# Performance work log

Measured on AMD Instinct MI355X. Metric: run time of the kernel, lower is better.

The kernel has to match this reference:

```python
import jax, jax.numpy as jnp
import numpy as np

NUM_USERS = 100000
NUM_ITEMS = 200000
N = NUM_USERS + NUM_ITEMS
D = 64
NNZ = 5_000_000
B = 16384
N_LAYERS = 3


def setup_inputs() -> dict:
    key = jax.random.key(0)
    ks = jax.random.split(key, 7)
    users = jax.random.randint(ks[0], (B,), 0, NUM_USERS, dtype=jnp.int32)
    items = jax.random.randint(ks[1], (B,), 0, NUM_ITEMS, dtype=jnp.int32)
    edge_row = jax.random.randint(ks[2], (NNZ,), 0, N, dtype=jnp.int32)
    edge_col = jax.random.randint(ks[3], (NNZ,), 0, N, dtype=jnp.int32)
    # mimic D^-1/2 A D^-1/2 normalization scale (~1/avg_degree)
    edge_vals = jax.random.uniform(ks[4], (NNZ,), dtype=jnp.float32) * 0.06
    user_emb = jax.random.normal(ks[5], (NUM_USERS, D), dtype=jnp.float32) * 0.1
    item_emb = jax.random.normal(ks[6], (NUM_ITEMS, D), dtype=jnp.float32) * 0.1
    return {
        "users": users, "items": items,
        "edge_row": edge_row, "edge_col": edge_col, "edge_vals": edge_vals,
        "user_emb": user_emb, "item_emb": item_emb,
        "n_layers": N_LAYERS,
    }


def _spmm(edge_row, edge_col, edge_vals, x):
    # sparse [N,N] @ dense [N,D] via gather + segment_sum
    msg = x[edge_col] * edge_vals[:, None]  # [nnz, D]
    return jax.ops.segment_sum(msg, edge_row, num_segments=N)


def reference(users, items, edge_row, edge_col, edge_vals, user_emb, item_emb, n_layers):
    # LightGCN.computer(): propagate + mean over layers (running-sum form)
    all_emb = jnp.concatenate([user_emb, item_emb], axis=0)  # [N, D]
    acc = all_emb
    for _ in range(n_layers):
        all_emb = _spmm(edge_row, edge_col, edge_vals, all_emb)
        acc = acc + all_emb
    light_out = acc / (n_layers + 1)
    all_users = light_out[:NUM_USERS]
    all_items = light_out[NUM_USERS:]
    # forward(users, items): elementwise dot product
    users_emb = all_users[users]
    items_emb = all_items[items]
    gamma = jnp.sum(users_emb * items_emb, axis=1)  # [B]
    return gamma
```

## Files before the change

kernel.cpp:

```cpp
#include <hip/hip_runtime.h>
#include <hip/hip_fp16.h>
#include <hip/hip_fp8.h>

namespace {

constexpr int kUsers = 100000;
constexpr int kItems = 200000;
constexpr int kN     = kUsers + kItems;
constexpr int kD     = 64;
constexpr int kNNZ   = 5000000;
constexpr int kB     = 16384;
constexpr int kRowsPerBkt = 2048;
constexpr int kNBKT  = (kN + kRowsPerBkt - 1) / kRowsPerBkt;
constexpr int kSEPB  = 4096;
constexpr int kCap   = 40960;
constexpr int kMaxSub = 2 * kB;

typedef int   v2i __attribute__((ext_vector_type(2)));
typedef float v4f __attribute__((ext_vector_type(4)));

#if defined(__has_builtin)
#if __has_builtin(__builtin_amdgcn_cvt_pk_f32_fp8) && __has_builtin(__builtin_amdgcn_cvt_f32_fp8)
#define NATIVE_FP8 1
#endif
#endif
#ifndef NATIVE_FP8
#define NATIVE_FP8 0
#endif

constexpr float kValScale = NATIVE_FP8 ? 1.0f : 256.0f;

__device__ inline void dec8(v2i h, float* f) {
#if NATIVE_FP8
  auto a0 = __builtin_amdgcn_cvt_pk_f32_fp8(h.x, false);
  auto a1 = __builtin_amdgcn_cvt_pk_f32_fp8(h.x, true);
  auto a2 = __builtin_amdgcn_cvt_pk_f32_fp8(h.y, false);
  auto a3 = __builtin_amdgcn_cvt_pk_f32_fp8(h.y, true);
  f[0] = a0[0]; f[1] = a0[1]; f[2] = a1[0]; f[3] = a1[1];
  f[4] = a2[0]; f[5] = a2[1]; f[6] = a3[0]; f[7] = a3[1];
#else
  unsigned int ws[2] = {(unsigned int)h.x, (unsigned int)h.y};
#pragma unroll
  for (int q = 0; q < 2; ++q) {
    unsigned int w = ws[q];
    unsigned int a = ((w & 0x007f007fu) << 7) | ((w & 0x00800080u) << 8);
    unsigned int b = (((w >> 8) & 0x007f007fu) << 7) | (((w >> 8) & 0x00800080u) << 8);
    float2 e = __half22float2(*reinterpret_cast<const __half2*>(&a));
    float2 o = __half22float2(*reinterpret_cast<const __half2*>(&b));
    f[4 * q + 0] = e.x; f[4 * q + 1] = o.x; f[4 * q + 2] = e.y; f[4 * q + 3] = o.y;
  }
#endif
}

__device__ inline float dec1(unsigned char b) {
#if NATIVE_FP8
  return __builtin_amdgcn_cvt_f32_fp8((int)b, 0) * 0.015625f;
#else
  unsigned int hb = ((b & 0x7fu) << 7) | ((b & 0x80u) << 8);
  return __half2float(__ushort_as_half((unsigned short)hb)) * 4.0f;
#endif
}

__device__ inline unsigned char enc(float f) { __hip_fp8_e4m3 q(f); return q.__x; }

__device__ inline float vdec(int w) {
  return __half2float(__ushort_as_half((unsigned short)((w >> 17) & 0x7FFC))) * kValScale;
}

__global__ void zero3(int* __restrict__ gpos, int* __restrict__ mark,
                      int* __restrict__ scnt) {
  int i = blockIdx.x * blockDim.x + threadIdx.x;
  if (i < kN) mark[i] = 0;
  if (i < kNBKT + 1) gpos[i] = 0;
  if (i == 0) scnt[0] = 0;
}

__global__ void bucket_scatter(const int* __restrict__ row, const int* __restrict__ col,
                               const float* __restrict__ val, int* __restrict__ gpos,
                               int* __restrict__ tmp4, unsigned short* __restrict__ tmpr) {
  __shared__ int hcnt[4][kNBKT];
  __shared__ int lofs[kNBKT];
  __shared__ int hbase[kNBKT];
  __shared__ int lds[256];
  __shared__ int sp[kSEPB];
  __shared__ unsigned short sr[kSEPB];
  __shared__ unsigned short sb[kSEPB];
  int t = threadIdx.x;
  int wv = t >> 6;
  long base = (long)blockIdx.x * kSEPB;
  int valid = (int)min((long)kSEPB, (long)kNNZ - base);
  for (int i = t; i < kNBKT; i += 256) {
    hcnt[0][i] = 0; hcnt[1][i] = 0; hcnt[2][i] = 0; hcnt[3][i] = 0;
  }
  __syncthreads();
  int py[16], bk[16], rl[16], rk[16];
  bool ok[16];
#pragma unroll
  for (int j = 0; j < 16; ++j) {
    long i = base + j * 256 + t;
    ok[j] = (i < kNNZ);
    if (ok[j]) {
      int r = __builtin_nontemporal_load(row + i);
      int c = __builtin_nontemporal_load(col + i);
      float v = __builtin_nontemporal_load(val + i);
      bk[j] = r >> 11;
      rl[j] = r & 2047;
      unsigned short hb = __half_as_ushort(__float2half_rn(v));
      int v13 = ((int)hb + 2) >> 2;
      py[j] = c | (v13 << 19);
      rk[j] = atomicAdd(&hcnt[wv][bk[j]], 1);
    }
  }
  __syncthreads();
  int own = 0;
  if (t < kNBKT) {
    int c0 = hcnt[0][t], c1 = hcnt[1][t], c2 = hcnt[2][t], c3 = hcnt[3][t];
    hcnt[0][t] = 0; hcnt[1][t] = c0; hcnt[2][t] = c0 + c1; hcnt[3][t] = c0 + c1 + c2;
    own = c0 + c1 + c2 + c3;
  }
  lds[t] = own;
  __syncthreads();
  for (int o = 1; o < 256; o <<= 1) {
    int x = (t >= o) ? lds[t - o] : 0;
    __syncthreads();
    if (t >= o) lds[t] += x;
    __syncthreads();
  }
  if (t < kNBKT) {
    lofs[t] = lds[t] - own;
    hbase[t] = t * kCap + atomicAdd(&gpos[t], own);
  }
  __syncthreads();
#pragma unroll
  for (int j = 0; j < 16; ++j) {
    if (ok[j]) {
      int pos = lofs[bk[j]] + hcnt[wv][bk[j]] + rk[j];
      sp[pos] = py[j];
      sr[pos] = (unsigned short)rl[j];
      sb[pos] = (unsigned short)bk[j];
    }
  }
  __syncthreads();
#pragma unroll
  for (int j = 0; j < 16; ++j) {
    int pos = t + j * 256;
    if (pos < valid) {
      int b = sb[pos];
      int w = hbase[b] + (pos - lofs[b]);
      tmp4[w] = sp[pos];
      tmpr[w] = sr[pos];
    }
  }
}

__global__ __launch_bounds__(1024) void build_csr(
    const int* __restrict__ gpos, const int* __restrict__ tmp4,
    const unsigned short* __restrict__ tmpr, int* __restrict__ rowptr,
    int* __restrict__ edges) {
  __shared__ int h[kRowsPerBkt];
  __shared__ int lsum[256];
  __shared__ int gscan[256];
  int b = blockIdx.x >> 1;
  int half = blockIdx.x & 1;
  int t = threadIdx.x;
  if (t < 256) gscan[t] = (t < kNBKT) ? gpos[t] : 0;
  for (int i = t; i < kRowsPerBkt; i += 1024) h[i] = 0;
  __syncthreads();
  for (int o = 1; o < 256; o <<= 1) {
    int v = 0;
    if (t < 256 && t >= o) v = gscan[t - o];
    __syncthreads();
    if (t < 256 && t >= o) gscan[t] += v;
    __syncthreads();
  }
  int bucket_base = (b == 0) ? 0 : gscan[b - 1];
  int s = b * kCap;
  int e = s + gpos[b];
  for (int j = s + t; j < e; j += 1024) atomicAdd(&h[tmpr[j]], 1);
  __syncthreads();
  int cnt[8], pref[8];
  if (t < 256) {
    int acc = 0;
#pragma unroll
    for (int k = 0; k < 8; ++k) {
      cnt[k] = h[t * 8 + k];
      pref[k] = acc;
      acc += cnt[k];
    }
    lsum[t] = acc;
  }
  __syncthreads();
  for (int o = 1; o < 256; o <<= 1) {
    int v = 0;
    if (t < 256 && t >= o) v = lsum[t - o];
    __syncthreads();
    if (t < 256 && t >= o) lsum[t] += v;
    __syncthreads();
  }
  if (t < 256) {
    int ex = (t == 0) ? 0 : lsum[t - 1];
#pragma unroll
    for (int k = 0; k < 8; ++k) {
      int g = bucket_base + ex + pref[k];
      int r = b * kRowsPerBkt + t * 8 + k;
      if (half == 0 && r < kN) rowptr[r] = g;
      h[t * 8 + k] = g;
    }
  }
  if (blockIdx.x == 0 && t == 0) rowptr[kN] = kNNZ;
  __syncthreads();
  int lo = half << 10, hi = lo + 1024;
  for (int j = s + t; j < e; j += 1024) {
    int rl = tmpr[j];
    if (rl >= lo && rl < hi) {
      int dst = atomicAdd(&h[rl], 1);
      edges[dst] = tmp4[j];
    }
  }
}

__global__ void mark_rows(const int* __restrict__ users, const int* __restrict__ items,
                          int* __restrict__ mark) {
  int i = blockIdx.x * blockDim.x + threadIdx.x;
  if (i >= kB) return;
  mark[users[i]] = 1;
  mark[kUsers + items[i]] = 1;
}

__global__ void compact_rows(const int* __restrict__ mark, int* __restrict__ list,
                             int* __restrict__ cnt) {
  __shared__ int wbase[4];
  int t = threadIdx.x;
  int i = blockIdx.x * 256 + t;
  bool m = (i < kN) && mark[i];
  unsigned long long bal = __ballot(m);
  int wv = t >> 6, ln = t & 63;
  if (ln == 0) wbase[wv] = __popcll(bal);
  __syncthreads();
  if (t == 0) {
    int tot = wbase[0] + wbase[1] + wbase[2] + wbase[3];
    int base = tot ? atomicAdd(cnt, tot) : 0;
    int p = base;
#pragma unroll
    for (int w = 0; w < 4; ++w) { int c = wbase[w]; wbase[w] = p; p += c; }
  }
  __syncthreads();
  if (m) {
    int rank = __popcll(bal & ((1ull << ln) - 1));
    list[wbase[wv] + rank] = i;
  }
}

__global__ void mark_cols(const int* __restrict__ list, const int* __restrict__ cnt,
                          const int* __restrict__ rowptr, const int* __restrict__ edges,
                          int* __restrict__ mark) {
  int p = blockIdx.x * blockDim.x + threadIdx.x;
  if (p >= *cnt) return;
  int r = list[p];
  int s = rowptr[r], e = rowptr[r + 1];
  for (int j = s; j < e; ++j) mark[edges[j] & 0x7FFFF] = 1;
}

__global__ void to_fp8(const float* __restrict__ ue, const float* __restrict__ ie,
                       unsigned char* __restrict__ xq) {
  int t = blockIdx.x * blockDim.x + threadIdx.x;
  if (t >= kN * kD / 8) return;
  int row = t >> 3;
  int seg = t & 7;
  const float* src = (row < kUsers) ? (ue + (size_t)row * kD + seg * 8)
                                    : (ie + (size_t)(row - kUsers) * kD + seg * 8);
  v4f a = __builtin_nontemporal_load((const v4f*)src);
  v4f b = __builtin_nontemporal_load((const v4f*)src + 1);
  float f[8] = {a.x, a.y, a.z, a.w, b.x, b.y, b.z, b.w};
  unsigned int w0 = 0, w1 = 0;
#pragma unroll
  for (int k = 0; k < 4; ++k) w0 |= (unsigned int)enc(f[k] * 64.f) << (8 * k);
#pragma unroll
  for (int k = 0; k < 4; ++k) w1 |= (unsigned int)enc(f[4 + k] * 64.f) << (8 * k);
  v2i o; o.x = (int)w0; o.y = (int)w1;
  ((v2i*)xq)[t] = o;
}

template <int MODE>
__global__ __launch_bounds__(256, 8) void spmm(
    const int* __restrict__ rowptr, const int* __restrict__ edges,
    const unsigned char* __restrict__ x, unsigned char* __restrict__ yq,
    const int* __restrict__ aux, const int* __restrict__ cnt) {
  int t = threadIdx.x;
  int l = t & 7;
  int wid = (blockIdx.x * 256 + t) >> 6;
  int g = (t >> 3) & 7;
  int p = wid * 8 + g;
  int r = -1;
  bool live = false;
  if (MODE == 2) {
    int n = *cnt;
    if (p < n) { r = aux[p]; live = true; }
  } else {
    if (p < kN) { r = p; live = (MODE == 0) || (aux[r] != 0); }
  }
  int s = 0, e = 0;
  if (live) { s = rowptr[r]; e = rowptr[r + 1]; }
  int mx = e - s;
#pragma unroll
  for (int m = 8; m <= 32; m <<= 1) mx = max(mx, __shfl_xor(mx, m, 64));
  float acc[8];
#pragma unroll
  for (int k = 0; k < 8; ++k) acc[k] = 0.f;
  int last = max(e - 1, 0);
  int j = s;
  int E0 = edges[min(j, last)];
  int E1 = edges[min(j + 1, last)];
  int E2 = edges[min(j + 2, last)];
  int E3 = edges[min(j + 3, last)];
  for (int it = 0; it < mx; it += 4) {
    float v0 = (j     < e) ? vdec(E0) : 0.f;
    float v1 = (j + 1 < e) ? vdec(E1) : 0.f;
    float v2 = (j + 2 < e) ? vdec(E2) : 0.f;
    float v3 = (j + 3 < e) ? vdec(E3) : 0.f;
    v2i h0 = ((const v2i*)(x + (size_t)(E0 & 0x7FFFF) * kD))[l];
    v2i h1 = ((const v2i*)(x + (size_t)(E1 & 0x7FFFF) * kD))[l];
    v2i h2 = ((const v2i*)(x + (size_t)(E2 & 0x7FFFF) * kD))[l];
    v2i h3 = ((const v2i*)(x + (size_t)(E3 & 0x7FFFF) * kD))[l];
    j += 4;
    E0 = edges[min(j, last)];
    E1 = edges[min(j + 1, last)];
    E2 = edges[min(j + 2, last)];
    E3 = edges[min(j + 3, last)];
    float f[8];
    dec8(h0, f);
#pragma unroll
    for (int k = 0; k < 8; ++k) acc[k] = fmaf(v0, f[k], acc[k]);
    dec8(h1, f);
#pragma unroll
    for (int k = 0; k < 8; ++k) acc[k] = fmaf(v1, f[k], acc[k]);
    dec8(h2, f);
#pragma unroll
    for (int k = 0; k < 8; ++k) acc[k] = fmaf(v2, f[k], acc[k]);
    dec8(h3, f);
#pragma unroll
    for (int k = 0; k < 8; ++k) acc[k] = fmaf(v3, f[k], acc[k]);
  }
  if (live) {
    unsigned int w0 = 0, w1 = 0;
#pragma unroll
    for (int k = 0; k < 4; ++k) w0 |= (unsigned int)enc(acc[k]) << (8 * k);
#pragma unroll
    for (int k = 0; k < 4; ++k) w1 |= (unsigned int)enc(acc[4 + k]) << (8 * k);
    v2i o; o.x = (int)w0; o.y = (int)w1;
    ((v2i*)yq)[(size_t)r * 8 + l] = o;
  }
}

__global__ void finalize(const int* __restrict__ users, const int* __restrict__ items,
                         const float* __restrict__ uemb, const float* __restrict__ iemb,
                         const unsigned char* __restrict__ l1,
                         const unsigned char* __restrict__ l2,
                         const unsigned char* __restrict__ l3, float* __restrict__ out) {
  int tid = blockIdx.x * blockDim.x + threadIdx.x;
  if (tid >= kB * kD) return;
  int b = tid >> 6, d = tid & 63;
  size_t u = (size_t)users[b] * kD + d;
  size_t iw = (size_t)(kUsers + items[b]) * kD + d;
  float us = uemb[(size_t)users[b] * kD + d] + dec1(l1[u]) + dec1(l2[u]) + dec1(l3[u]);
  float vs = iemb[(size_t)items[b] * kD + d] + dec1(l1[iw]) + dec1(l2[iw]) + dec1(l3[iw]);
  float p = us * vs;
  for (int o = 32; o > 0; o >>= 1) p += __shfl_down(p, o, 64);
  if (d == 0) out[b] = p * 0.0625f;
}

}

extern "C" void kernel_launch(void* const* d_in, const int* in_sizes, int n_in,
                              void* d_out, int out_size, void* d_ws, size_t ws_size,
                              hipStream_t stream) {
  const int*   users = (const int*)d_in[0];
  const int*   items = (const int*)d_in[1];
  const int*   erow  = (const int*)d_in[2];
  const int*   ecol  = (const int*)d_in[3];
  const float* evals = (const float*)d_in[4];
  const float* uemb  = (const float*)d_in[5];
  const float* iemb  = (const float*)d_in[6];
  float* out = (float*)d_out;

  char* ws = (char*)d_ws;
  size_t off = 0;
  auto take = [&](size_t bytes) -> char* {
    char* p = ws + off;
    off = (off + bytes + 255) & ~(size_t)255;
    return p;
  };
  int*    rowptr   = (int*)take((size_t)(kN + 1) * 4);
  int*    gpos     = (int*)take((kNBKT + 1) * 4);
  int*    mark     = (int*)take((size_t)kN * 4);
  int*    list     = (int*)take((size_t)kMaxSub * 4);
  int*    scnt     = (int*)take(256);
  int*    edges    = (int*)take((size_t)kNNZ * 4);
  int*    tmp4     = (int*)take((size_t)kNBKT * kCap * 4);
  unsigned short* tmpr = (unsigned short*)take((size_t)kNBKT * kCap * 2);
  unsigned char* xq0 = (unsigned char*)take((size_t)kN * kD);
  unsigned char* xq1 = (unsigned char*)take((size_t)kN * kD);
  unsigned char* xq2 = (unsigned char*)take((size_t)kN * kD);
  (void)ws_size; (void)in_sizes; (void)n_in; (void)out_size;

  const int nScatBlocks = (kNNZ + kSEPB - 1) / kSEPB;
  const int nSpmmBlocks = (kN + 31) / 32;
  const int nSubBlocks  = (kMaxSub + 31) / 32;
  const int nRowBlocks  = (kN + 255) / 256;

  zero3<<<nRowBlocks, 256, 0, stream>>>(gpos, mark, scnt);
  bucket_scatter<<<nScatBlocks, 256, 0, stream>>>(erow, ecol, evals, gpos, tmp4, tmpr);
  build_csr<<<2 * kNBKT, 1024, 0, stream>>>(gpos, tmp4, tmpr, rowptr, edges);

  mark_rows<<<(kB + 255) / 256, 256, 0, stream>>>(users, items, mark);
  compact_rows<<<nRowBlocks, 256, 0, stream>>>(mark, list, scnt);
  mark_cols<<<(kMaxSub + 255) / 256, 256, 0, stream>>>(list, scnt, rowptr, edges, mark);

  to_fp8<<<(kN * kD / 8 + 255) / 256, 256, 0, stream>>>(uemb, iemb, xq0);
  spmm<0><<<nSpmmBlocks, 256, 0, stream>>>(rowptr, edges, xq0, xq1, nullptr, nullptr);
  spmm<1><<<nSpmmBlocks, 256, 0, stream>>>(rowptr, edges, xq1, xq2, mark, nullptr);
  spmm<2><<<nSubBlocks, 256, 0, stream>>>(rowptr, edges, xq2, xq0, list, scnt);
  finalize<<<(kB * kD) / 256, 256, 0, stream>>>(users, items, uemb, iemb,
                                                xq1, xq2, xq0, out);
}
```

Before: 460.7 us.

## Merge small setup kernels into larger launches and halve build_csr histogram work

Folds the zero, mark_rows, compact_rows, mark_cols and fp8-conversion kernels into extra blocks of the neighbouring launches: prep, bucket_scatter, build_csr and spmm<0>. This cuts the launch count and lets independent work overlap within one grid. build_csr now builds a histogram for only its own half of each bucket, using a 1024-entry shared array, and writes rowptr from both halves. Risk: mark_cols now runs concurrently with spmm<0> rather than before it, which is only valid because spmm<0> does not read mark.

```diff
diff --git a/kernel.cpp b/kernel.cpp
--- a/kernel.cpp
+++ b/kernel.cpp
@@ -16,6 +16,15 @@
 constexpr int kCap   = 40960;
 constexpr int kMaxSub = 2 * kB;
 
+constexpr int kZeroBlocks  = (kN + 255) / 256;
+constexpr int kFp8Blocks   = (kN * kD / 8 + 255) / 256;
+constexpr int kScatBlocks  = (kNNZ + kSEPB - 1) / kSEPB;
+constexpr int kMarkBlocks  = (kB + 255) / 256;
+constexpr int kBuildBlocks = 2 * kNBKT;
+constexpr int kCompBlocks  = (kN + 1023) / 1024;
+constexpr int kSpmmMain    = (kN + 31) / 32;
+constexpr int kMCBlocks    = kMaxSub / 256;
+
 typedef int   v2i __attribute__((ext_vector_type(2)));
 typedef float v4f __attribute__((ext_vector_type(4)));
 
@@ -67,17 +76,48 @@
   return __half2float(__ushort_as_half((unsigned short)((w >> 17) & 0x7FFC))) * kValScale;
 }
 
-__global__ void zero3(int* __restrict__ gpos, int* __restrict__ mark,
-                      int* __restrict__ scnt) {
-  int i = blockIdx.x * blockDim.x + threadIdx.x;
-  if (i < kN) mark[i] = 0;
-  if (i < kNBKT + 1) gpos[i] = 0;
-  if (i == 0) scnt[0] = 0;
+__global__ void prep(int* __restrict__ gpos, int* __restrict__ mark,
+                     int* __restrict__ scnt, const float* __restrict__ ue,
+                     const float* __restrict__ ie, unsigned char* __restrict__ xq) {
+  int bid = blockIdx.x;
+  if (bid < kZeroBlocks) {
+    int i = bid * 256 + threadIdx.x;
+    if (i < kN) mark[i] = 0;
+    if (i < kNBKT + 1) gpos[i] = 0;
+    if (i == 0) scnt[0] = 0;
+    return;
+  }
+  int t = (bid - kZeroBlocks) * 256 + threadIdx.x;
+  if (t >= kN * kD / 8) return;
+  int row = t >> 3;
+  int seg = t & 7;
+  const float* src = (row < kUsers) ? (ue + (size_t)row * kD + seg * 8)
+                                    : (ie + (size_t)(row - kUsers) * kD + seg * 8);
+  v4f a = __builtin_nontemporal_load((const v4f*)src);
+  v4f b = __builtin_nontemporal_load((const v4f*)src + 1);
+  float f[8] = {a.x, a.y, a.z, a.w, b.x, b.y, b.z, b.w};
+  unsigned int w0 = 0, w1 = 0;
+#pragma unroll
+  for (int k = 0; k < 4; ++k) w0 |= (unsigned int)enc(f[k] * 64.f) << (8 * k);
+#pragma unroll
+  for (int k = 0; k < 4; ++k) w1 |= (unsigned int)enc(f[4 + k] * 64.f) << (8 * k);
+  v2i o; o.x = (int)w0; o.y = (int)w1;
+  ((v2i*)xq)[t] = o;
 }
 
 __global__ void bucket_scatter(const int* __restrict__ row, const int* __restrict__ col,
                                const float* __restrict__ val, int* __restrict__ gpos,
-                               int* __restrict__ tmp4, unsigned short* __restrict__ tmpr) {
+                               int* __restrict__ tmp4, unsigned short* __restrict__ tmpr,
+                               const int* __restrict__ users, const int* __restrict__ items,
+                               int* __restrict__ mark) {
+  if ((int)blockIdx.x >= kScatBlocks) {
+    int i = ((int)blockIdx.x - kScatBlocks) * 256 + threadIdx.x;
+    if (i < kB) {
+      mark[users[i]] = 1;
+      mark[kUsers + items[i]] = 1;
+    }
+    return;
+  }
   __shared__ int hcnt[4][kNBKT];
   __shared__ int lofs[kNBKT];
   __shared__ int hbase[kNBKT];
@@ -156,15 +196,39 @@
 __global__ __launch_bounds__(1024) void build_csr(
     const int* __restrict__ gpos, const int* __restrict__ tmp4,
     const unsigned short* __restrict__ tmpr, int* __restrict__ rowptr,
-    int* __restrict__ edges) {
-  __shared__ int h[kRowsPerBkt];
+    int* __restrict__ edges, const int* __restrict__ mark,
+    int* __restrict__ list, int* __restrict__ scnt) {
+  int t = threadIdx.x;
+  if ((int)blockIdx.x >= kBuildBlocks) {
+    __shared__ int wbase[16];
+    int i = ((int)blockIdx.x - kBuildBlocks) * 1024 + t;
+    bool m = (i < kN) && mark[i];
+    unsigned long long bal = __ballot(m);
+    int wv = t >> 6, ln = t & 63;
+    if (ln == 0) wbase[wv] = __popcll(bal);
+    __syncthreads();
+    if (t == 0) {
+      int tot = 0;
+#pragma unroll
+      for (int w = 0; w < 16; ++w) tot += wbase[w];
+      int p = tot ? atomicAdd(scnt, tot) : 0;
+#pragma unroll
+      for (int w = 0; w < 16; ++w) { int c = wbase[w]; wbase[w] = p; p += c; }
+    }
+    __syncthreads();
+    if (m) {
+      int rank = __popcll(bal & ((1ull << ln) - 1));
+      list[wbase[wv] + rank] = i;
+    }
+    return;
+  }
+  __shared__ int h[1024];
   __shared__ int lsum[256];
   __shared__ int gscan[256];
   int b = blockIdx.x >> 1;
   int half = blockIdx.x & 1;
-  int t = threadIdx.x;
   if (t < 256) gscan[t] = (t < kNBKT) ? gpos[t] : 0;
-  for (int i = t; i < kRowsPerBkt; i += 1024) h[i] = 0;
+  if (t < 1024) h[t] = 0;
   __syncthreads();
   for (int o = 1; o < 256; o <<= 1) {
     int v = 0;
@@ -176,14 +240,18 @@
   int bucket_base = (b == 0) ? 0 : gscan[b - 1];
   int s = b * kCap;
   int e = s + gpos[b];
-  for (int j = s + t; j < e; j += 1024) atomicAdd(&h[tmpr[j]], 1);
-  __syncthreads();
-  int cnt[8], pref[8];
+  int lo = half << 10, hi = lo + 1024;
+  for (int j = s + t; j < e; j += 1024) {
+    int rl = tmpr[j];
+    if (rl >= lo && rl < hi) atomicAdd(&h[rl - lo], 1);
+  }
+  __syncthreads();
+  int cnt[4], pref[4];
   if (t < 256) {
     int acc = 0;
 #pragma unroll
-    for (int k = 0; k < 8; ++k) {
-      cnt[k] = h[t * 8 + k];
+    for (int k = 0; k < 4; ++k) {
+      cnt[k] = h[t * 4 + k];
       pref[k] = acc;
       acc += cnt[k];
     }
@@ -197,95 +265,43 @@
     if (t < 256 && t >= o) lsum[t] += v;
     __syncthreads();
   }
+  int base_local = half ? (gpos[b] - lsum[255]) : 0;
   if (t < 256) {
     int ex = (t == 0) ? 0 : lsum[t - 1];
 #pragma unroll
-    for (int k = 0; k < 8; ++k) {
-      int g = bucket_base + ex + pref[k];
-      int r = b * kRowsPerBkt + t * 8 + k;
-      if (half == 0 && r < kN) rowptr[r] = g;
-      h[t * 8 + k] = g;
+    for (int k = 0; k < 4; ++k) {
+      int g = bucket_base + base_local + ex + pref[k];
+      int r = b * kRowsPerBkt + lo + t * 4 + k;
+      if (r < kN) rowptr[r] = g;
+      h[t * 4 + k] = g;
     }
   }
   if (blockIdx.x == 0 && t == 0) rowptr[kN] = kNNZ;
   __syncthreads();
-  int lo = half << 10, hi = lo + 1024;
   for (int j = s + t; j < e; j += 1024) {
     int rl = tmpr[j];
     if (rl >= lo && rl < hi) {
-      int dst = atomicAdd(&h[rl], 1);
+      int dst = atomicAdd(&h[rl - lo], 1);
       edges[dst] = tmp4[j];
     }
   }
-}
-
-__global__ void mark_rows(const int* __restrict__ users, const int* __restrict__ items,
-                          int* __restrict__ mark) {
-  int i = blockIdx.x * blockDim.x + threadIdx.x;
-  if (i >= kB) return;
-  mark[users[i]] = 1;
-  mark[kUsers + items[i]] = 1;
-}
-
-__global__ void compact_rows(const int* __restrict__ mark, int* __restrict__ list,
-                             int* __restrict__ cnt) {
-  __shared__ int wbase[4];
-  int t = threadIdx.x;
-  int i = blockIdx.x * 256 + t;
-  bool m = (i < kN) && mark[i];
-  unsigned long long bal = __ballot(m);
-  int wv = t >> 6, ln = t & 63;
-  if (ln == 0) wbase[wv] = __popcll(bal);
-  __syncthreads();
-  if (t == 0) {
-    int tot = wbase[0] + wbase[1] + wbase[2] + wbase[3];
-    int base = tot ? atomicAdd(cnt, tot) : 0;
-    int p = base;
-#pragma unroll
-    for (int w = 0; w < 4; ++w) { int c = wbase[w]; wbase[w] = p; p += c; }
-  }
-  __syncthreads();
-  if (m) {
-    int rank = __popcll(bal & ((1ull << ln) - 1));
-    list[wbase[wv] + rank] = i;
-  }
-}
-
-__global__ void mark_cols(const int* __restrict__ list, const int* __restrict__ cnt,
-                          const int* __restrict__ rowptr, const int* __restrict__ edges,
-                          int* __restrict__ mark) {
-  int p = blockIdx.x * blockDim.x + threadIdx.x;
-  if (p >= *cnt) return;
-  int r = list[p];
-  int s = rowptr[r], e = rowptr[r + 1];
-  for (int j = s; j < e; ++j) mark[edges[j] & 0x7FFFF] = 1;
-}
-
-__global__ void to_fp8(const float* __restrict__ ue, const float* __restrict__ ie,
-                       unsigned char* __restrict__ xq) {
-  int t = blockIdx.x * blockDim.x + threadIdx.x;
-  if (t >= kN * kD / 8) return;
-  int row = t >> 3;
-  int seg = t & 7;
-  const float* src = (row < kUsers) ? (ue + (size_t)row * kD + seg * 8)
-                                    : (ie + (size_t)(row - kUsers) * kD + seg * 8);
-  v4f a = __builtin_nontemporal_load((const v4f*)src);
-  v4f b = __builtin_nontemporal_load((const v4f*)src + 1);
-  float f[8] = {a.x, a.y, a.z, a.w, b.x, b.y, b.z, b.w};
-  unsigned int w0 = 0, w1 = 0;
-#pragma unroll
-  for (int k = 0; k < 4; ++k) w0 |= (unsigned int)enc(f[k] * 64.f) << (8 * k);
-#pragma unroll
-  for (int k = 0; k < 4; ++k) w1 |= (unsigned int)enc(f[4 + k] * 64.f) << (8 * k);
-  v2i o; o.x = (int)w0; o.y = (int)w1;
-  ((v2i*)xq)[t] = o;
 }
 
 template <int MODE>
 __global__ __launch_bounds__(256, 8) void spmm(
     const int* __restrict__ rowptr, const int* __restrict__ edges,
     const unsigned char* __restrict__ x, unsigned char* __restrict__ yq,
-    const int* __restrict__ aux, const int* __restrict__ cnt) {
+    const int* __restrict__ aux, const int* __restrict__ cnt,
+    int* __restrict__ mcmark) {
+  if (MODE == 0 && (int)blockIdx.x >= kSpmmMain) {
+    int p = ((int)blockIdx.x - kSpmmMain) * 256 + threadIdx.x;
+    if (p < *cnt) {
+      int r = aux[p];
+      int s = rowptr[r], e = rowptr[r + 1];
+      for (int j = s; j < e; ++j) mcmark[edges[j] & 0x7FFFF] = 1;
+    }
+    return;
+  }
   int t = threadIdx.x;
   int l = t & 7;
   int wid = (blockIdx.x * 256 + t) >> 6;
@@ -403,23 +419,16 @@
   unsigned char* xq2 = (unsigned char*)take((size_t)kN * kD);
   (void)ws_size; (void)in_sizes; (void)n_in; (void)out_size;
 
-  const int nScatBlocks = (kNNZ + kSEPB - 1) / kSEPB;
-  const int nSpmmBlocks = (kN + 31) / 32;
-  const int nSubBlocks  = (kMaxSub + 31) / 32;
-  const int nRowBlocks  = (kN + 255) / 256;
-
-  zero3<<<nRowBlocks, 256, 0, stream>>>(gpos, mark, scnt);
-  bucket_scatter<<<nScatBlocks, 256, 0, stream>>>(erow, ecol, evals, gpos, tmp4, tmpr);
-  build_csr<<<2 * kNBKT, 1024, 0, stream>>>(gpos, tmp4, tmpr, rowptr, edges);
-
-  mark_rows<<<(kB + 255) / 256, 256, 0, stream>>>(users, items, mark);
-  compact_rows<<<nRowBlocks, 256, 0, stream>>>(mark, list, scnt);
-  mark_cols<<<(kMaxSub + 255) / 256, 256, 0, stream>>>(list, scnt, rowptr, edges, mark);
-
-  to_fp8<<<(kN * kD / 8 + 255) / 256, 256, 0, stream>>>(uemb, iemb, xq0);
-  spmm<0><<<nSpmmBlocks, 256, 0, stream>>>(rowptr, edges, xq0, xq1, nullptr, nullptr);
-  spmm<1><<<nSpmmBlocks, 256, 0, stream>>>(rowptr, edges, xq1, xq2, mark, nullptr);
-  spmm<2><<<nSubBlocks, 256, 0, stream>>>(rowptr, edges, xq2, xq0, list, scnt);
+  prep<<<kZeroBlocks + kFp8Blocks, 256, 0, stream>>>(gpos, mark, scnt, uemb, iemb, xq0);
+  bucket_scatter<<<kScatBlocks + kMarkBlocks, 256, 0, stream>>>(
+      erow, ecol, evals, gpos, tmp4, tmpr, users, items, mark);
+  build_csr<<<kBuildBlocks + kCompBlocks, 1024, 0, stream>>>(
+      gpos, tmp4, tmpr, rowptr, edges, mark, list, scnt);
+  spmm<0><<<kSpmmMain + kMCBlocks, 256, 0, stream>>>(rowptr, edges, xq0, xq1,
+                                                     list, scnt, mark);
+  spmm<1><<<kSpmmMain, 256, 0, stream>>>(rowptr, edges, xq1, xq2, mark, nullptr, nullptr);
+  spmm<2><<<(kMaxSub + 31) / 32, 256, 0, stream>>>(rowptr, edges, xq2, xq0,
+                                                   list, scnt, nullptr);
   finalize<<<(kB * kD) / 256, 256, 0, stream>>>(users, items, uemb, iemb,
                                                 xq1, xq2, xq0, out);
 }
```

Measured after the change: 441.0 us. 1.04x faster.
